# Kernel optimization log

Hardware: AMD Instinct MI355X
Metric: run time of the kernel (lower is better)

## Reference

```python
import jax, jax.numpy as jnp
import numpy as np
from jax import lax

# Mamba hyperparameters (match init_kwargs / mamba_ssm defaults)
D_MODEL = 256
D_STATE = 16
D_CONV = 4
EXPAND = 2
D_INNER = EXPAND * D_MODEL          # 512
DT_RANK = (D_MODEL + 15) // 16      # ceil(d_model/16) = 16, mamba 'auto'
B, T, N = 2, 128, 64
LN_EPS = 1e-5


def setup_inputs() -> dict:
    key = jax.random.key(0)
    ks = jax.random.split(key, 8)
    s = 0.02
    return {
        "x": jax.random.normal(ks[0], (B, T, N, D_MODEL), jnp.float32),
        # Mamba params (mamba_ssm defaults: in_proj/out_proj no bias, conv bias, dt_proj bias)
        "W_in": jax.random.normal(ks[1], (2 * D_INNER, D_MODEL), jnp.float32) * s,
        "W_conv": jax.random.normal(ks[2], (D_INNER, 1, D_CONV), jnp.float32) * s,
        "b_conv": jnp.zeros((D_INNER,), jnp.float32),
        "W_xproj": jax.random.normal(ks[3], (DT_RANK + 2 * D_STATE, D_INNER), jnp.float32) * s,
        "W_dt": jax.random.normal(ks[4], (D_INNER, DT_RANK), jnp.float32) * s,
        "b_dt": jax.random.normal(ks[5], (D_INNER,), jnp.float32) * 0.1,
        "A_log": jnp.log(jnp.tile(jnp.arange(1, D_STATE + 1, dtype=jnp.float32), (D_INNER, 1))),
        "D_param": jnp.ones((D_INNER,), jnp.float32),
        "W_out": jax.random.normal(ks[6], (D_MODEL, D_INNER), jnp.float32) * s,
        # LayerNorm
        "gamma": jnp.ones((D_MODEL,), jnp.float32),
        "beta": jnp.zeros((D_MODEL,), jnp.float32),
    }


def _mamba_block(xr, W_in, W_conv, b_conv, W_xproj, W_dt, b_dt, A_log, D_param, W_out):
    # xr: (BN, T, D_MODEL)
    xz = xr @ W_in.T                                   # (BN, T, 2*D_INNER)
    xp, z = jnp.split(xz, 2, axis=-1)
    # causal depthwise conv over time
    xc = lax.conv_general_dilated(
        xp.transpose(0, 2, 1), W_conv, (1,), [(D_CONV - 1, 0)],
        dimension_numbers=("NCH", "OIH", "NCH"), feature_group_count=D_INNER)
    u = jax.nn.silu(xc + b_conv[None, :, None]).transpose(0, 2, 1)  # (BN, T, D_INNER)
    x_dbl = u @ W_xproj.T                              # (BN, T, DT_RANK + 2*D_STATE)
    dt_raw = x_dbl[..., :DT_RANK]
    Bm = x_dbl[..., DT_RANK:DT_RANK + D_STATE]         # (BN, T, D_STATE)
    Cm = x_dbl[..., DT_RANK + D_STATE:]                # (BN, T, D_STATE)
    dt = jax.nn.softplus(dt_raw @ W_dt.T + b_dt)       # (BN, T, D_INNER)
    A = -jnp.exp(A_log)                                # (D_INNER, D_STATE)

    def step(h, inps):
        dt_t, B_t, C_t, u_t = inps                     # (BN,DI),(BN,DS),(BN,DS),(BN,DI)
        dA = jnp.exp(dt_t[..., None] * A)              # (BN, DI, DS)
        h = h * dA + dt_t[..., None] * B_t[:, None, :] * u_t[..., None]
        y = jnp.einsum("bds,bs->bd", h, C_t)
        return h, y

    BN = xr.shape[0]
    h0 = jnp.zeros((BN, D_INNER, D_STATE), xr.dtype)
    xs = (dt.transpose(1, 0, 2), Bm.transpose(1, 0, 2),
          Cm.transpose(1, 0, 2), u.transpose(1, 0, 2))
    _, ys = lax.scan(step, h0, xs)                     # ys: (T, BN, D_INNER)
    y = ys.transpose(1, 0, 2) + u * D_param            # skip term D*u
    y = y * jax.nn.silu(z)                             # gated output
    return y @ W_out.T                                 # (BN, T, D_MODEL)


def reference(x, W_in, W_conv, b_conv, W_xproj, W_dt, b_dt, A_log, D_param, W_out, gamma, beta):
    B_, T_, N_, Dm = x.shape
    xr = x.transpose(0, 2, 1, 3).reshape(B_ * N_, T_, Dm)
    out = _mamba_block(xr, W_in, W_conv, b_conv, W_xproj, W_dt, b_dt, A_log, D_param, W_out)
    # LayerNorm over D
    mu = out.mean(-1, keepdims=True)
    var = out.var(-1, keepdims=True)
    out = (out - mu) / jnp.sqrt(var + LN_EPS) * gamma + beta
    # dropout is identity in eval mode
    return out.reshape(B_, N_, T_, Dm).transpose(0, 2, 1, 3)
```

## Files before the change

kernel.cpp:

```cpp
#include <hip/hip_runtime.h>

typedef short bf16x8 __attribute__((ext_vector_type(8)));
typedef float f32x4 __attribute__((ext_vector_type(4)));

__device__ __forceinline__ unsigned short f2bf(float f) {
    unsigned int u = __builtin_bit_cast(unsigned int, f);
    u = (u + 0x7FFFu + ((u >> 16) & 1u)) >> 16;
    return (unsigned short)u;
}
__device__ __forceinline__ float bf2f(unsigned short h) {
    unsigned int u = ((unsigned int)h) << 16;
    return __builtin_bit_cast(float, u);
}
__device__ __forceinline__ float dot4(f32x4 a, f32x4 b) {
    return a[0] * b[0] + a[1] * b[1] + a[2] * b[2] + a[3] * b[3];
}

__global__ __launch_bounds__(256) void k_prep_x(const float* __restrict__ x,
                                                unsigned int* __restrict__ Xbf2) {
    int tid = blockIdx.x * 256 + threadIdx.x;
    int c4 = tid & 63;
    int r  = tid >> 6;
    int t = r & 127, bn = r >> 7;
    int n = bn & 63, b = bn >> 6;
    const float4 v = *((const float4*)(x + ((((size_t)(b * 128 + t)) * 64 + n) << 8)) + c4);
    uint2 o;
    o.x = (unsigned int)f2bf(v.x) | ((unsigned int)f2bf(v.y) << 16);
    o.y = (unsigned int)f2bf(v.z) | ((unsigned int)f2bf(v.w) << 16);
    *((uint2*)(Xbf2 + ((size_t)r << 7)) + c4) = o;
}

__global__ __launch_bounds__(256) void k_f2bf(const float* __restrict__ in,
                                              unsigned int* __restrict__ out, int n4) {
    int tid = blockIdx.x * 256 + threadIdx.x;
    if (tid >= n4) return;
    float4 v = ((const float4*)in)[tid];
    uint2 o;
    o.x = (unsigned int)f2bf(v.x) | ((unsigned int)f2bf(v.y) << 16);
    o.y = (unsigned int)f2bf(v.z) | ((unsigned int)f2bf(v.w) << 16);
    ((uint2*)out)[tid] = o;
}

__global__ __launch_bounds__(256, 2) void k_gemm1(const unsigned short* __restrict__ A,
                                                  const unsigned short* __restrict__ Bw,
                                                  unsigned short* __restrict__ xp,
                                                  unsigned short* __restrict__ z) {
    __shared__ unsigned short As[2][128][64];
    __shared__ unsigned short Bs[2][128][64];
    const int tid = threadIdx.x;
    const int l = tid & 63, w = tid >> 6;
    const int lr = l & 15, lg = l >> 4;
    const int wr = w >> 1, wc = w & 1;
    const int row0 = blockIdx.x * 128;
    const int n0b  = blockIdx.y * 128;

    bf16x8 sa[4], sb[4];
    auto LOAD = [&](int k0) {
        #pragma unroll
        for (int r2 = 0; r2 < 4; ++r2) {
            int cc = tid + r2 * 256;
            int row = cc >> 3, ke = (cc & 7) * 8;
            sa[r2] = *(const bf16x8*)(A  + (size_t)(row0 + row) * 256 + k0 + ke);
            sb[r2] = *(const bf16x8*)(Bw + (size_t)(n0b + row) * 256 + k0 + ke);
        }
    };
    auto WRITE = [&](int buf) {
        #pragma unroll
        for (int r2 = 0; r2 < 4; ++r2) {
            int cc = tid + r2 * 256;
            int row = cc >> 3, ke = (cc & 7) * 8;
            int ks = ke ^ ((row & 7) * 8);
            *(bf16x8*)&As[buf][row][ks] = sa[r2];
            *(bf16x8*)&Bs[buf][row][ks] = sb[r2];
        }
    };

    f32x4 acc[4][4] = {};
    LOAD(0); WRITE(0);
    __syncthreads();
    int cur = 0;
    for (int kt = 0; kt < 4; ++kt) {
        if (kt < 3) LOAD((kt + 1) * 64);
        #pragma unroll
        for (int ks = 0; ks < 2; ++ks) {
            const int ka = ks * 32;
            bf16x8 a[4], b[4];
            #pragma unroll
            for (int mi = 0; mi < 4; ++mi) {
                int row = wr * 64 + mi * 16 + lr;
                int e = (ka + lg * 8) ^ ((row & 7) * 8);
                a[mi] = *(const bf16x8*)&As[cur][row][e];
            }
            #pragma unroll
            for (int ni = 0; ni < 4; ++ni) {
                int row = wc * 64 + ni * 16 + lr;
                int e = (ka + lg * 8) ^ ((row & 7) * 8);
                b[ni] = *(const bf16x8*)&Bs[cur][row][e];
            }
            #pragma unroll
            for (int mi = 0; mi < 4; ++mi)
                #pragma unroll
                for (int ni = 0; ni < 4; ++ni)
                    acc[mi][ni] = __builtin_amdgcn_mfma_f32_16x16x32_bf16(a[mi], b[ni], acc[mi][ni], 0, 0, 0);
        }
        if (kt < 3) WRITE(cur ^ 1);
        __syncthreads();
        cur ^= 1;
    }
    const bool isz = (blockIdx.y >= 4);
    unsigned short* dst = isz ? z : xp;
    const int colbase = (blockIdx.y - (isz ? 4 : 0)) * 128 + wc * 64;
    #pragma unroll
    for (int mi = 0; mi < 4; ++mi)
        #pragma unroll
        for (int r = 0; r < 4; ++r) {
            const int row = row0 + wr * 64 + mi * 16 + lg * 4 + r;
            #pragma unroll
            for (int ni = 0; ni < 4; ++ni)
                dst[(size_t)row * 512 + colbase + ni * 16 + lr] = f2bf(acc[mi][ni][r]);
        }
}

__global__ __launch_bounds__(256) void k_conv(const unsigned short* __restrict__ xp,
                                              const float* __restrict__ Wc,
                                              const float* __restrict__ bcv,
                                              unsigned int* __restrict__ ub2) {
    int tid = blockIdx.x * 256 + threadIdx.x;
    int d2 = tid & 255, r = tid >> 8;
    int t = r & 127, bn = r >> 7;
    int d = d2 << 1;
    const unsigned short* src = xp + (size_t)bn * 65536 + d;
    f32x4 wa = *(const f32x4*)(Wc + d * 4);
    f32x4 wb = *(const f32x4*)(Wc + d * 4 + 4);
    float a0 = bcv[d], a1 = bcv[d + 1];
    #pragma unroll
    for (int k = 0; k < 4; ++k) {
        int tt = t - 3 + k;
        if (tt >= 0) {
            unsigned int p = *(const unsigned int*)(src + (size_t)tt * 512);
            a0 += bf2f((unsigned short)(p & 0xFFFFu)) * wa[k];
            a1 += bf2f((unsigned short)(p >> 16)) * wb[k];
        }
    }
    float u0 = a0 / (1.f + __expf(-a0));
    float u1 = a1 / (1.f + __expf(-a1));
    ub2[((size_t)bn * 65536 + (size_t)t * 512 + d) >> 1] =
        (unsigned int)f2bf(u0) | ((unsigned int)f2bf(u1) << 16);
}

__global__ __launch_bounds__(256, 2) void k_xproj(const unsigned short* __restrict__ U,
                                                  const unsigned short* __restrict__ Wb,
                                                  float* __restrict__ xdbl) {
    const int w = threadIdx.x >> 6, l = threadIdx.x & 63;
    const int lr = l & 15, lg = l >> 4;
    const int row0 = blockIdx.x * 64 + w * 16;
    f32x4 acc[3] = {};
    for (int k0 = 0; k0 < 512; k0 += 32) {
        const int ka = k0 + lg * 8;
        bf16x8 a = *(const bf16x8*)(U + (size_t)(row0 + lr) * 512 + ka);
        bf16x8 b[3];
        #pragma unroll
        for (int ni = 0; ni < 3; ++ni)
            b[ni] = *(const bf16x8*)(Wb + (size_t)(ni * 16 + lr) * 512 + ka);
        #pragma unroll
        for (int ni = 0; ni < 3; ++ni)
            acc[ni] = __builtin_amdgcn_mfma_f32_16x16x32_bf16(a, b[ni], acc[ni], 0, 0, 0);
    }
    #pragma unroll
    for (int r = 0; r < 4; ++r) {
        const int row = row0 + lg * 4 + r;
        #pragma unroll
        for (int ni = 0; ni < 3; ++ni)
            xdbl[(size_t)row * 48 + ni * 16 + lr] = acc[ni][r];
    }
}

__global__ __launch_bounds__(512, 2) void k_scan(const float* __restrict__ xdbl,
                                                 const unsigned short* __restrict__ ub,
                                                 const unsigned short* __restrict__ zb,
                                                 const float* __restrict__ W_dt,
                                                 const float* __restrict__ b_dt,
                                                 const float* __restrict__ A_log,
                                                 const float* __restrict__ Dp,
                                                 unsigned short* __restrict__ yb) {
    __shared__ float bc[128][48];
    __shared__ _Float16 dtS[128][128];
    __shared__ _Float16 cP[3][16][128];
    __shared__ _Float16 cH[3][16][128];
    const int bn = blockIdx.x >> 2;
    const int d0 = (blockIdx.x & 3) * 128;
    {
        const float* src = xdbl + (size_t)(bn * 128) * 48;
        #pragma unroll
        for (int k = 0; k < 3; ++k) {
            int li = threadIdx.x + k * 512;
            int row = li / 12, c4 = li - row * 12;
            *(f32x4*)(&bc[row][c4 * 4]) = *(const f32x4*)(src + row * 48 + c4 * 4);
        }
    }
    const int dg = threadIdx.x & 127;
    const int c  = threadIdx.x >> 7;
    const int d  = d0 + dg;
    bool fast = true;
    #pragma unroll
    for (int j = 0; j < 16; ++j) {
        float aj = __expf(A_log[d * 16 + j]);
        fast = fast && (fabsf(aj - (float)(j + 1)) < 1e-3f * (float)(j + 1));
    }
    f32x4 wd0 = *(const f32x4*)(W_dt + d * 16);
    f32x4 wd1 = *(const f32x4*)(W_dt + d * 16 + 4);
    f32x4 wd2 = *(const f32x4*)(W_dt + d * 16 + 8);
    f32x4 wd3 = *(const f32x4*)(W_dt + d * 16 + 12);
    const float dbias = b_dt[d];
    const unsigned short* up = ub + (size_t)bn * 65536 + d;
    const unsigned short* zp = zb + (size_t)bn * 65536 + d;
    unsigned short* yp = yb + (size_t)bn * 65536 + d;
    const int t0 = c * 32;
    __syncthreads();
    #pragma unroll 1
    for (int i = 0; i < 32; ++i) {
        const int t = t0 + i;
        float dl = dbias
                 + dot4(wd0, *(const f32x4*)&bc[t][0])
                 + dot4(wd1, *(const f32x4*)&bc[t][4])
                 + dot4(wd2, *(const f32x4*)&bc[t][8])
                 + dot4(wd3, *(const f32x4*)&bc[t][12]);
        float dt = (dl > 20.f) ? dl : __logf(1.f + __expf(dl));
        dtS[t][dg] = (_Float16)dt;
    }
    float h[16], p[16];
    #pragma unroll
    for (int j = 0; j < 16; ++j) { h[j] = 0.f; p[j] = 1.f; }
    if (c < 3) {
        if (fast) {
            float S = 1.f;
            #pragma unroll 1
            for (int i = 0; i < 32; ++i) {
                const int t = t0 + i;
                float dtv = (float)dtS[t][dg];
                float du  = dtv * bf2f(up[t * 512]);
                float E = __expf(-dtv);
                S *= E;
                float E2 = E * E, E3 = E2 * E, E4 = E2 * E2;
                float E8 = E4 * E4, E12 = E8 * E4;
                f32x4 B0 = *(const f32x4*)&bc[t][16];
                f32x4 B1 = *(const f32x4*)&bc[t][20];
                f32x4 B2 = *(const f32x4*)&bc[t][24];
                f32x4 B3 = *(const f32x4*)&bc[t][28];
                h[0]  = h[0]  * E         + du * B0[0];
                h[1]  = h[1]  * E2        + du * B0[1];
                h[2]  = h[2]  * E3        + du * B0[2];
                h[3]  = h[3]  * E4        + du * B0[3];
                h[4]  = h[4]  * (E4 * E)  + du * B1[0];
                h[5]  = h[5]  * (E4 * E2) + du * B1[1];
                h[6]  = h[6]  * (E4 * E3) + du * B1[2];
                h[7]  = h[7]  * E8        + du * B1[3];
                h[8]  = h[8]  * (E8 * E)  + du * B2[0];
                h[9]  = h[9]  * (E8 * E2) + du * B2[1];
                h[10] = h[10] * (E8 * E3) + du * B2[2];
                h[11] = h[11] * E12       + du * B2[3];
                h[12] = h[12] * (E12 * E) + du * B3[0];
                h[13] = h[13] * (E12 * E2)+ du * B3[1];
                h[14] = h[14] * (E12 * E3)+ du * B3[2];
                h[15] = h[15] * (E12 * E4)+ du * B3[3];
            }
            float S2 = S * S, S3 = S2 * S, S4 = S2 * S2;
            float S8 = S4 * S4, S12 = S8 * S4;
            p[0] = S;        p[1] = S2;        p[2] = S3;        p[3] = S4;
            p[4] = S4 * S;   p[5] = S4 * S2;   p[6] = S4 * S3;   p[7] = S8;
            p[8] = S8 * S;   p[9] = S8 * S2;   p[10] = S8 * S3;  p[11] = S12;
            p[12] = S12 * S; p[13] = S12 * S2; p[14] = S12 * S3; p[15] = S12 * S4;
        } else {
            #pragma unroll 1
            for (int i = 0; i < 32; ++i) {
                const int t = t0 + i;
                float dtv = (float)dtS[t][dg];
                float du  = dtv * bf2f(up[t * 512]);
                #pragma unroll
                for (int j = 0; j < 16; ++j) {
                    float e = __expf(-dtv * __expf(A_log[d * 16 + j]));
                    h[j] = h[j] * e + du * bc[t][16 + j];
                    p[j] *= e;
                }
            }
        }
        #pragma unroll
        for (int s = 0; s < 16; ++s) {
            cP[c][s][dg] = (_Float16)p[s];
            cH[c][s][dg] = (_Float16)h[s];
        }
    }
    __syncthreads();
    #pragma unroll
    for (int s = 1; s < 4; s <<= 1) {
        const bool act = (c >= s) && (c < 3);
        __syncthreads();
        if (act) {
            #pragma unroll
            for (int g = 0; g < 4; ++g) {
                #pragma unroll
                for (int k = 0; k < 4; ++k) {
                    const int j = 4 * g + k;
                    float gv = (float)cH[c - s][j][dg];
                    float qv = (float)cP[c - s][j][dg];
                    h[j] += p[j] * gv;
                    p[j] *= qv;
                }
            }
        }
        __syncthreads();
        if (act) {
            #pragma unroll
            for (int j = 0; j < 16; ++j) {
                cP[c][j][dg] = (_Float16)p[j];
                cH[c][j][dg] = (_Float16)h[j];
            }
        }
    }
    __syncthreads();
    #pragma unroll
    for (int j = 0; j < 16; ++j) h[j] = 0.f;
    if (c > 0) {
        #pragma unroll
        for (int j = 0; j < 16; ++j) h[j] = (float)cH[c - 1][j][dg];
    }
    const float dpar = Dp[d];
    if (fast) {
        #pragma unroll 1
        for (int i = 0; i < 32; ++i) {
            const int t = t0 + i;
            float dtv = (float)dtS[t][dg];
            float uv  = bf2f(up[t * 512]);
            float zv  = bf2f(zp[t * 512]);
            float du = dtv * uv;
            float E = __expf(-dtv);
            float E2 = E * E, E3 = E2 * E, E4 = E2 * E2;
            float E8 = E4 * E4, E12 = E8 * E4;
            f32x4 B0 = *(const f32x4*)&bc[t][16];
            f32x4 B1 = *(const f32x4*)&bc[t][20];
            f32x4 B2 = *(const f32x4*)&bc[t][24];
            f32x4 B3 = *(const f32x4*)&bc[t][28];
            f32x4 C0 = *(const f32x4*)&bc[t][32];
            f32x4 C1 = *(const f32x4*)&bc[t][36];
            f32x4 C2 = *(const f32x4*)&bc[t][40];
            f32x4 C3 = *(const f32x4*)&bc[t][44];
            h[0]  = h[0]  * E         + du * B0[0];
            h[1]  = h[1]  * E2        + du * B0[1];
            h[2]  = h[2]  * E3        + du * B0[2];
            h[3]  = h[3]  * E4        + du * B0[3];
            h[4]  = h[4]  * (E4 * E)  + du * B1[0];
            h[5]  = h[5]  * (E4 * E2) + du * B1[1];
            h[6]  = h[6]  * (E4 * E3) + du * B1[2];
            h[7]  = h[7]  * E8        + du * B1[3];
            h[8]  = h[8]  * (E8 * E)  + du * B2[0];
            h[9]  = h[9]  * (E8 * E2) + du * B2[1];
            h[10] = h[10] * (E8 * E3) + du * B2[2];
            h[11] = h[11] * E12       + du * B2[3];
            h[12] = h[12] * (E12 * E) + du * B3[0];
            h[13] = h[13] * (E12 * E2)+ du * B3[1];
            h[14] = h[14] * (E12 * E3)+ du * B3[2];
            h[15] = h[15] * (E12 * E4)+ du * B3[3];
            float y0 = h[0] * C0[0] + h[1] * C0[1] + h[2] * C0[2] + h[3] * C0[3];
            float y1 = h[4] * C1[0] + h[5] * C1[1] + h[6] * C1[2] + h[7] * C1[3];
            float y2 = h[8] * C2[0] + h[9] * C2[1] + h[10] * C2[2] + h[11] * C2[3];
            float y3 = h[12] * C3[0] + h[13] * C3[1] + h[14] * C3[2] + h[15] * C3[3];
            float y = (y0 + y1) + (y2 + y3);
            float yf = (y + uv * dpar) * (zv / (1.f + __expf(-zv)));
            yp[t * 512] = f2bf(yf);
        }
    } else {
        #pragma unroll 1
        for (int i = 0; i < 32; ++i) {
            const int t = t0 + i;
            float dtv = (float)dtS[t][dg];
            float uv  = bf2f(up[t * 512]);
            float zv  = bf2f(zp[t * 512]);
            float du = dtv * uv;
            float y = 0.f;
            #pragma unroll
            for (int j = 0; j < 16; ++j) {
                float e = __expf(-dtv * __expf(A_log[d * 16 + j]));
                h[j] = h[j] * e + du * bc[t][16 + j];
                y += h[j] * bc[t][32 + j];
            }
            float yf = (y + uv * dpar) * (zv / (1.f + __expf(-zv)));
            yp[t * 512] = f2bf(yf);
        }
    }
}

__global__ __launch_bounds__(256, 2) void k_out_ln(const unsigned short* __restrict__ Y,
                                                   const unsigned short* __restrict__ Wb,
                                                   const float* __restrict__ gamma,
                                                   const float* __restrict__ beta,
                                                   float* __restrict__ out) {
    __shared__ float s_sum[32], s_sq[32];
    const int w = threadIdx.x >> 6, l = threadIdx.x & 63;
    const int lr = l & 15, lg = l >> 4;
    const int row0 = blockIdx.x * 32;
    const int n0 = w * 64;
    f32x4 acc[2][4] = {};
    for (int k0 = 0; k0 < 512; k0 += 32) {
        const int ka = k0 + lg * 8;
        bf16x8 a[2], b[4];
        #pragma unroll
        for (int mi = 0; mi < 2; ++mi)
            a[mi] = *(const bf16x8*)(Y + (size_t)(row0 + mi * 16 + lr) * 512 + ka);
        #pragma unroll
        for (int ni = 0; ni < 4; ++ni)
            b[ni] = *(const bf16x8*)(Wb + (size_t)(n0 + ni * 16 + lr) * 512 + ka);
        #pragma unroll
        for (int mi = 0; mi < 2; ++mi)
            #pragma unroll
            for (int ni = 0; ni < 4; ++ni)
                acc[mi][ni] = __builtin_amdgcn_mfma_f32_16x16x32_bf16(a[mi], b[ni], acc[mi][ni], 0, 0, 0);
    }
    if (threadIdx.x < 32) { s_sum[threadIdx.x] = 0.f; s_sq[threadIdx.x] = 0.f; }
    __syncthreads();
    #pragma unroll
    for (int mi = 0; mi < 2; ++mi)
        #pragma unroll
        for (int r = 0; r < 4; ++r) {
            float s = 0.f, q = 0.f;
            #pragma unroll
            for (int ni = 0; ni < 4; ++ni) { float v = acc[mi][ni][r]; s += v; q += v * v; }
            #pragma unroll
            for (int m = 1; m < 16; m <<= 1) { s += __shfl_xor(s, m, 64); q += __shfl_xor(q, m, 64); }
            if (lr == 0) {
                atomicAdd(&s_sum[mi * 16 + lg * 4 + r], s);
                atomicAdd(&s_sq[mi * 16 + lg * 4 + r], q);
            }
        }
    __syncthreads();
    float g[4], be[4];
    #pragma unroll
    for (int ni = 0; ni < 4; ++ni) {
        g[ni] = gamma[n0 + ni * 16 + lr];
        be[ni] = beta[n0 + ni * 16 + lr];
    }
    #pragma unroll
    for (int mi = 0; mi < 2; ++mi)
        #pragma unroll
        for (int r = 0; r < 4; ++r) {
            const int rl = mi * 16 + lg * 4 + r;
            const int row = row0 + rl;
            const float mu = s_sum[rl] * (1.f / 256.f);
            const float var = s_sq[rl] * (1.f / 256.f) - mu * mu;
            const float rs = rsqrtf(var + 1e-5f);
            const int t = row & 127, bn = row >> 7;
            const int nn = bn & 63, bb = bn >> 6;
            float* orow = out + ((((size_t)(bb * 128 + t)) * 64 + nn) << 8);
            #pragma unroll
            for (int ni = 0; ni < 4; ++ni)
                orow[n0 + ni * 16 + lr] = (acc[mi][ni][r] - mu) * rs * g[ni] + be[ni];
        }
}

extern "C" void kernel_launch(void* const* d_in, const int* in_sizes, int n_in,
                              void* d_out, int out_size, void* d_ws, size_t ws_size,
                              hipStream_t stream) {
    const float* x      = (const float*)d_in[0];
    const float* W_in   = (const float*)d_in[1];
    const float* W_conv = (const float*)d_in[2];
    const float* b_conv = (const float*)d_in[3];
    const float* W_xprj = (const float*)d_in[4];
    const float* W_dt   = (const float*)d_in[5];
    const float* b_dt   = (const float*)d_in[6];
    const float* A_log  = (const float*)d_in[7];
    const float* D_par  = (const float*)d_in[8];
    const float* W_out  = (const float*)d_in[9];
    const float* gamma  = (const float*)d_in[10];
    const float* beta   = (const float*)d_in[11];
    float* out = (float*)d_out;

    char* ws = (char*)d_ws;
    size_t off = 0;
    auto alloc = [&](size_t bytes) -> void* {
        void* p = ws + off;
        off += (bytes + 255) & ~(size_t)255;
        return p;
    };
    unsigned short* Xbf   = (unsigned short*)alloc(16384ull * 256 * 2);
    unsigned short* Winb  = (unsigned short*)alloc(1024ull * 256 * 2);
    unsigned short* Wxpb  = (unsigned short*)alloc(48ull * 512 * 2);
    unsigned short* xp    = (unsigned short*)alloc(16384ull * 512 * 2);
    unsigned short* Woutb = (unsigned short*)alloc(256ull * 512 * 2);
    unsigned short* zb    = (unsigned short*)alloc(16384ull * 512 * 2);
    unsigned short* ub    = (unsigned short*)alloc(16384ull * 512 * 2);
    float*          xdbl  = (float*)alloc(16384ull * 48 * 4);
    unsigned short* yb    = (unsigned short*)alloc(16384ull * 512 * 2);
    if (off > ws_size) return;

    k_prep_x<<<4096, 256, 0, stream>>>(x, (unsigned int*)Xbf);
    k_f2bf<<<256, 256, 0, stream>>>(W_in, (unsigned int*)Winb, 65536);
    k_f2bf<<<24, 256, 0, stream>>>(W_xprj, (unsigned int*)Wxpb, 6144);
    k_f2bf<<<128, 256, 0, stream>>>(W_out, (unsigned int*)Woutb, 32768);
    k_gemm1<<<dim3(128, 8), 256, 0, stream>>>(Xbf, Winb, xp, zb);
    k_conv<<<16384, 256, 0, stream>>>(xp, W_conv, b_conv, (unsigned int*)ub);
    k_xproj<<<256, 256, 0, stream>>>(ub, Wxpb, xdbl);
    k_scan<<<512, 512, 0, stream>>>(xdbl, ub, zb, W_dt, b_dt, A_log, D_par, yb);
    k_out_ln<<<512, 256, 0, stream>>>(yb, Woutb, gamma, beta, out);
}
```

Before: 139.1 us.

## Fuse causal depthwise conv and SiLU into in-projection GEMM epilogue

After: 125.4 us. 1.11x faster.

```diff
diff --git a/kernel.cpp b/kernel.cpp
--- a/kernel.cpp
+++ b/kernel.cpp
@@ -30,23 +30,35 @@
     *((uint2*)(Xbf2 + ((size_t)r << 7)) + c4) = o;
 }
 
-__global__ __launch_bounds__(256) void k_f2bf(const float* __restrict__ in,
-                                              unsigned int* __restrict__ out, int n4) {
+__global__ __launch_bounds__(256) void k_f2bf3(const float* __restrict__ W_in,
+                                               const float* __restrict__ W_xp,
+                                               const float* __restrict__ W_out,
+                                               unsigned int* __restrict__ Winb,
+                                               unsigned int* __restrict__ Wxpb,
+                                               unsigned int* __restrict__ Woutb) {
     int tid = blockIdx.x * 256 + threadIdx.x;
-    if (tid >= n4) return;
-    float4 v = ((const float4*)in)[tid];
+    const float* src; unsigned int* dst; int idx;
+    if (tid < 65536)       { src = W_in;  dst = Winb;  idx = tid; }
+    else if (tid < 71680)  { src = W_xp;  dst = Wxpb;  idx = tid - 65536; }
+    else if (tid < 104448) { src = W_out; dst = Woutb; idx = tid - 71680; }
+    else return;
+    float4 v = ((const float4*)src)[idx];
     uint2 o;
     o.x = (unsigned int)f2bf(v.x) | ((unsigned int)f2bf(v.y) << 16);
     o.y = (unsigned int)f2bf(v.z) | ((unsigned int)f2bf(v.w) << 16);
-    ((uint2*)out)[tid] = o;
+    ((uint2*)dst)[idx] = o;
 }
 
 __global__ __launch_bounds__(256, 2) void k_gemm1(const unsigned short* __restrict__ A,
                                                   const unsigned short* __restrict__ Bw,
-                                                  unsigned short* __restrict__ xp,
+                                                  const float* __restrict__ Wc,
+                                                  const float* __restrict__ bcv,
+                                                  unsigned short* __restrict__ ub,
                                                   unsigned short* __restrict__ z) {
-    __shared__ unsigned short As[2][128][64];
-    __shared__ unsigned short Bs[2][128][64];
+    __shared__ char smem[65536];
+    unsigned short (*As)[128][64] = (unsigned short (*)[128][64])smem;
+    unsigned short (*Bs)[128][64] = (unsigned short (*)[128][64])(smem + 32768);
+    unsigned short (*xpS)[132]    = (unsigned short (*)[132])smem;
     const int tid = threadIdx.x;
     const int l = tid & 63, w = tid >> 6;
     const int lr = l & 15, lg = l >> 4;
@@ -107,45 +119,55 @@
         __syncthreads();
         cur ^= 1;
     }
-    const bool isz = (blockIdx.y >= 4);
-    unsigned short* dst = isz ? z : xp;
-    const int colbase = (blockIdx.y - (isz ? 4 : 0)) * 128 + wc * 64;
-    #pragma unroll
-    for (int mi = 0; mi < 4; ++mi)
-        #pragma unroll
-        for (int r = 0; r < 4; ++r) {
-            const int row = row0 + wr * 64 + mi * 16 + lg * 4 + r;
-            #pragma unroll
-            for (int ni = 0; ni < 4; ++ni)
-                dst[(size_t)row * 512 + colbase + ni * 16 + lr] = f2bf(acc[mi][ni][r]);
-        }
-}
-
-__global__ __launch_bounds__(256) void k_conv(const unsigned short* __restrict__ xp,
-                                              const float* __restrict__ Wc,
-                                              const float* __restrict__ bcv,
-                                              unsigned int* __restrict__ ub2) {
-    int tid = blockIdx.x * 256 + threadIdx.x;
-    int d2 = tid & 255, r = tid >> 8;
-    int t = r & 127, bn = r >> 7;
-    int d = d2 << 1;
-    const unsigned short* src = xp + (size_t)bn * 65536 + d;
-    f32x4 wa = *(const f32x4*)(Wc + d * 4);
-    f32x4 wb = *(const f32x4*)(Wc + d * 4 + 4);
-    float a0 = bcv[d], a1 = bcv[d + 1];
-    #pragma unroll
-    for (int k = 0; k < 4; ++k) {
-        int tt = t - 3 + k;
-        if (tt >= 0) {
-            unsigned int p = *(const unsigned int*)(src + (size_t)tt * 512);
-            a0 += bf2f((unsigned short)(p & 0xFFFFu)) * wa[k];
-            a1 += bf2f((unsigned short)(p >> 16)) * wb[k];
-        }
-    }
-    float u0 = a0 / (1.f + __expf(-a0));
-    float u1 = a1 / (1.f + __expf(-a1));
-    ub2[((size_t)bn * 65536 + (size_t)t * 512 + d) >> 1] =
-        (unsigned int)f2bf(u0) | ((unsigned int)f2bf(u1) << 16);
+    if (blockIdx.y >= 4) {
+        unsigned short* dst = z;
+        const int colbase = (blockIdx.y - 4) * 128 + wc * 64;
+        #pragma unroll
+        for (int mi = 0; mi < 4; ++mi)
+            #pragma unroll
+            for (int r = 0; r < 4; ++r) {
+                const int row = row0 + wr * 64 + mi * 16 + lg * 4 + r;
+                #pragma unroll
+                for (int ni = 0; ni < 4; ++ni)
+                    dst[(size_t)row * 512 + colbase + ni * 16 + lr] = f2bf(acc[mi][ni][r]);
+            }
+    } else {
+        #pragma unroll
+        for (int mi = 0; mi < 4; ++mi)
+            #pragma unroll
+            for (int r = 0; r < 4; ++r) {
+                const int trow = wr * 64 + mi * 16 + lg * 4 + r;
+                #pragma unroll
+                for (int ni = 0; ni < 4; ++ni)
+                    xpS[trow][wc * 64 + ni * 16 + lr] = f2bf(acc[mi][ni][r]);
+            }
+        __syncthreads();
+        const int d2 = tid & 63;
+        const int dloc = d2 << 1;
+        const int dglob = blockIdx.y * 128 + dloc;
+        f32x4 wa = *(const f32x4*)(Wc + dglob * 4);
+        f32x4 wb = *(const f32x4*)(Wc + dglob * 4 + 4);
+        const float b0 = bcv[dglob], b1 = bcv[dglob + 1];
+        unsigned int* dst = (unsigned int*)(ub + (size_t)blockIdx.x * 65536 + dglob);
+        const int tbase = tid >> 6;
+        #pragma unroll 1
+        for (int i = 0; i < 32; ++i) {
+            const int t = tbase + i * 4;
+            float a0 = b0, a1 = b1;
+            #pragma unroll
+            for (int k = 0; k < 4; ++k) {
+                int tt = t - 3 + k;
+                if (tt >= 0) {
+                    unsigned int pv = *(const unsigned int*)&xpS[tt][dloc];
+                    a0 += bf2f((unsigned short)(pv & 0xFFFFu)) * wa[k];
+                    a1 += bf2f((unsigned short)(pv >> 16)) * wb[k];
+                }
+            }
+            float u0 = a0 / (1.f + __expf(-a0));
+            float u1 = a1 / (1.f + __expf(-a1));
+            dst[(size_t)t * 256] = (unsigned int)f2bf(u0) | ((unsigned int)f2bf(u1) << 16);
+        }
+    }
 }
 
 __global__ __launch_bounds__(256, 2) void k_xproj(const unsigned short* __restrict__ U,
@@ -483,7 +505,6 @@
     unsigned short* Xbf   = (unsigned short*)alloc(16384ull * 256 * 2);
     unsigned short* Winb  = (unsigned short*)alloc(1024ull * 256 * 2);
     unsigned short* Wxpb  = (unsigned short*)alloc(48ull * 512 * 2);
-    unsigned short* xp    = (unsigned short*)alloc(16384ull * 512 * 2);
     unsigned short* Woutb = (unsigned short*)alloc(256ull * 512 * 2);
     unsigned short* zb    = (unsigned short*)alloc(16384ull * 512 * 2);
     unsigned short* ub    = (unsigned short*)alloc(16384ull * 512 * 2);
@@ -492,11 +513,10 @@
     if (off > ws_size) return;
 
     k_prep_x<<<4096, 256, 0, stream>>>(x, (unsigned int*)Xbf);
-    k_f2bf<<<256, 256, 0, stream>>>(W_in, (unsigned int*)Winb, 65536);
-    k_f2bf<<<24, 256, 0, stream>>>(W_xprj, (unsigned int*)Wxpb, 6144);
-    k_f2bf<<<128, 256, 0, stream>>>(W_out, (unsigned int*)Woutb, 32768);
-    k_gemm1<<<dim3(128, 8), 256, 0, stream>>>(Xbf, Winb, xp, zb);
-    k_conv<<<16384, 256, 0, stream>>>(xp, W_conv, b_conv, (unsigned int*)ub);
+    k_f2bf3<<<408, 256, 0, stream>>>(W_in, W_xprj, W_out,
+                                     (unsigned int*)Winb, (unsigned int*)Wxpb,
+                                     (unsigned int*)Woutb);
+    k_gemm1<<<dim3(128, 8), 256, 0, stream>>>(Xbf, Winb, W_conv, b_conv, ub, zb);
     k_xproj<<<256, 256, 0, stream>>>(ub, Wxpb, xdbl);
     k_scan<<<512, 512, 0, stream>>>(xdbl, ub, zb, W_dt, b_dt, A_log, D_par, yb);
     k_out_ln<<<512, 256, 0, stream>>>(yb, Woutb, gamma, beta, out);
```
